# Kernel optimization log

Hardware: AMD Instinct MI355X
Metric: run time of the kernel (lower is better)

The kernel has to match this reference:

```python
import jax, jax.numpy as jnp
import numpy as np

B, T, N, H = 1024, 256, 32, 64  # batch, SEQ_LEN, N_SERIES, RNN_HID_SIZE
EPS = 1e-05


def setup_inputs() -> dict:
    key = jax.random.key(0)
    ks = jax.random.split(key, 24)
    s_h = 1.0 / np.sqrt(H)
    s_n = 1.0 / np.sqrt(N)
    u = lambda k, shape, s: jax.random.uniform(k, shape, jnp.float32, -s, s)
    inp = {
        'values': jax.random.normal(ks[0], (B, T, N), jnp.float32),
        'masks': (jax.random.uniform(ks[1], (B, T, N)) < 0.8).astype(jnp.float32),
        'deltas': jax.random.uniform(ks[2], (B, T, N), jnp.float32) * 5.0,
        'evals': jax.random.normal(ks[3], (B, T, N), jnp.float32),
        'eval_masks': (jax.random.uniform(ks[4], (B, T, N)) < 0.1).astype(jnp.float32),
        'labels': (jax.random.uniform(ks[5], (B, 1)) < 0.5).astype(jnp.float32),
        'is_train': jnp.ones((B, 1), jnp.float32),
        # TemporalDecay h: Linear(N->H)
        'td_h_W': u(ks[6], (H, N), s_h), 'td_h_b': u(ks[7], (H,), s_h),
        # TemporalDecay x: diag Linear(N->N)
        'td_x_W': u(ks[8], (N, N), s_n), 'td_x_b': u(ks[9], (N,), s_n),
        # hist_reg: Linear(H->N)
        'hist_W': u(ks[10], (N, H), s_n), 'hist_b': u(ks[11], (N,), s_n),
        # feat_reg: masked Linear(N->N), mask = 1 - I
        'feat_W': u(ks[12], (N, N), s_n), 'feat_b': u(ks[13], (N,), s_n),
        # weight_combine: Linear(2N->N)
        'wc_W': u(ks[14], (N, 2 * N), s_n), 'wc_b': u(ks[15], (N,), s_n),
        # LSTMCell(2N -> H)
        'W_ih': u(ks[16], (4 * H, 2 * N), s_h), 'W_hh': u(ks[17], (4 * H, H), s_h),
        'b_ih': u(ks[18], (4 * H,), s_h), 'b_hh': u(ks[19], (4 * H,), s_h),
        # out: Linear(H->1)
        'out_W': u(ks[20], (1, H), s_h), 'out_b': u(ks[21], (1,), s_h),
    }
    return inp


def _rits_forward(values, masks, deltas, labels, is_train,
                  td_h_W, td_h_b, td_x_W, td_x_b, hist_W, hist_b,
                  feat_W, feat_b, wc_W, wc_b, W_ih, W_hh, b_ih, b_hh,
                  out_W, out_b):
    # time-major for scan: [T, B, N]
    vals_t = jnp.swapaxes(values, 0, 1)
    masks_t = jnp.swapaxes(masks, 0, 1)
    delts_t = jnp.swapaxes(deltas, 0, 1)

    feat_mask = 1.0 - jnp.eye(N, dtype=values.dtype)
    td_x_diag = jnp.diagonal(td_x_W)                  # W * eye(N) linear == elementwise diag

    def step(carry, xmd):
        h, c, x_loss = carry
        x, m, d = xmd
        gamma_h = jnp.exp(-jax.nn.relu(d @ td_h_W.T + td_h_b))   # [B,H]
        gamma_x = jnp.exp(-jax.nn.relu(d * td_x_diag + td_x_b))  # [B,N]
        h = h * gamma_h
        x_h = h @ hist_W.T + hist_b
        msum = jnp.sum(m) + EPS
        x_loss = x_loss + jnp.sum(jnp.abs(x - x_h) * m) / msum
        x_c = m * x + (1.0 - m) * x_h
        z_h = x_c @ (feat_W * feat_mask).T + feat_b
        x_loss = x_loss + jnp.sum(jnp.abs(x - z_h) * m) / msum
        alpha = jnp.concatenate([gamma_x, m], axis=1) @ wc_W.T + wc_b
        c_h = alpha * z_h + (1.0 - alpha) * x_h
        x_loss = x_loss + jnp.sum(jnp.abs(x - c_h) * m) / msum
        c_c = m * x + (1.0 - m) * c_h
        inputs = jnp.concatenate([c_c, m], axis=1)  # [B, 2N]
        gates = inputs @ W_ih.T + b_ih + h @ W_hh.T + b_hh
        i, f, g, o = jnp.split(gates, 4, axis=1)
        c = jax.nn.sigmoid(f) * c + jax.nn.sigmoid(i) * jnp.tanh(g)
        h = jax.nn.sigmoid(o) * jnp.tanh(c)
        return (h, c, x_loss), c_c

    h0 = jnp.zeros((values.shape[0], H), values.dtype)
    c0 = jnp.zeros((values.shape[0], H), values.dtype)
    (h, c, x_loss), imps = jax.lax.scan(step, (h0, c0, jnp.float32(0.0)),
                                        (vals_t, masks_t, delts_t))
    imputations = jnp.swapaxes(imps, 0, 1)  # [B, T, N]

    y_h = h @ out_W.T + out_b  # logits [B,1]
    # binary_cross_entropy_with_logits, reduce=False
    max_val = jnp.maximum(-y_h, 0.0)
    bce = y_h - y_h * labels + max_val + jnp.log(jnp.exp(-max_val) + jnp.exp(-y_h - max_val))
    y_loss = jnp.sum(bce * is_train) / (jnp.sum(is_train) + EPS)
    loss = x_loss / T + y_loss * 0.1
    predictions = jax.nn.sigmoid(y_h)
    return loss, predictions, imputations


def reference(values, masks, deltas, evals, eval_masks, labels, is_train,
              td_h_W, td_h_b, td_x_W, td_x_b, hist_W, hist_b, feat_W, feat_b,
              wc_W, wc_b, W_ih, W_hh, b_ih, b_hh, out_W, out_b):
    loss, predictions, imputations = _rits_forward(
        values, masks, deltas, labels, is_train,
        td_h_W, td_h_b, td_x_W, td_x_b, hist_W, hist_b,
        feat_W, feat_b, wc_W, wc_b, W_ih, W_hh, b_ih, b_hh, out_W, out_b)
    return loss, predictions, imputations
```

## Files before the change

kernel.cpp:

```cpp
#include <hip/hip_runtime.h>

#define EPSF 1e-5f

typedef _Float16 h2f  __attribute__((ext_vector_type(2)));
typedef _Float16 h8   __attribute__((ext_vector_type(8)));
typedef float    f32x4 __attribute__((ext_vector_type(4)));

#if defined(__has_builtin)
#if __has_builtin(__builtin_amdgcn_fdot2)
#define HAVE_FDOT2 1
#endif
#endif

__device__ __forceinline__ float fsig(float x){ return 1.0f/(1.0f+__expf(-x)); }
__device__ __forceinline__ float ftanh(float x){
  float e = __expf(2.f*x);
  float r = (e-1.f)/(e+1.f);
  return (x > 15.f) ? 1.f : ((x < -15.f) ? -1.f : r);
}
__device__ __forceinline__ int pkf(float lo, float hi){
  return __builtin_bit_cast(int, __builtin_amdgcn_cvt_pkrtz(lo, hi));
}
__device__ __forceinline__ int4 mk4(const float* p){
  return make_int4(pkf(p[0],p[1]),pkf(p[2],p[3]),pkf(p[4],p[5]),pkf(p[6],p[7]));
}
__device__ __forceinline__ float dot2(int w, int x, float acc){
#ifdef HAVE_FDOT2
  return __builtin_amdgcn_fdot2(__builtin_bit_cast(h2f, w),
                                __builtin_bit_cast(h2f, x), acc, false);
#else
  h2f a = __builtin_bit_cast(h2f, w), b = __builtin_bit_cast(h2f, x);
  return acc + (float)a[0]*(float)b[0] + (float)a[1]*(float)b[1];
#endif
}
__device__ __forceinline__ int rl_i(int v, int l){ return __builtin_amdgcn_readlane(v, l); }
__device__ __forceinline__ float rl_f(float v, int l){
  return __int_as_float(__builtin_amdgcn_readlane(__float_as_int(v), l));
}
#define MFMA(A,B,C) __builtin_amdgcn_mfma_f32_16x16x32_f16( \
    __builtin_bit_cast(h8,(A)), __builtin_bit_cast(h8,(B)), (C), 0,0,0)
#define BAR() do{ asm volatile("s_waitcnt lgkmcnt(0)" ::: "memory"); __builtin_amdgcn_s_barrier(); }while(0)

__global__ void msum_kernel(const float* __restrict__ masks, float* __restrict__ msum){
  const int t   = blockIdx.x;
  const int tid = threadIdx.x;
  const int b0  = tid >> 3;
  const int n4  = (tid & 7) << 2;
  float s = 0.f;
  #pragma unroll 4
  for (int i = 0; i < 32; ++i) {
    const int b = b0 + (i << 5);
    const float4 v = *reinterpret_cast<const float4*>(masks + ((size_t)b*256 + t)*32 + n4);
    s += v.x + v.y + v.z + v.w;
  }
  __shared__ float red[256];
  red[tid] = s; __syncthreads();
  for (int off = 128; off > 0; off >>= 1) {
    if (tid < off) red[tid] += red[tid + off];
    __syncthreads();
  }
  if (tid == 0) msum[t] = red[0] + EPSF;
}

__global__ __launch_bounds__(512)
__attribute__((amdgpu_waves_per_eu(2, 2)))
void rits_kernel(
  const float* __restrict__ values, const float* __restrict__ masks,
  const float* __restrict__ deltas, const float* __restrict__ labels,
  const float* __restrict__ is_train,
  const float* __restrict__ td_h_W, const float* __restrict__ td_h_b,
  const float* __restrict__ td_x_W, const float* __restrict__ td_x_b,
  const float* __restrict__ hist_W, const float* __restrict__ hist_b,
  const float* __restrict__ feat_W, const float* __restrict__ feat_b,
  const float* __restrict__ wc_W,  const float* __restrict__ wc_b,
  const float* __restrict__ W_ih,  const float* __restrict__ W_hh,
  const float* __restrict__ b_ih,  const float* __restrict__ b_hh,
  const float* __restrict__ out_W, const float* __restrict__ out_b,
  const float* __restrict__ msum,
  float* __restrict__ xl_acc, float* __restrict__ bce_acc,
  float* __restrict__ predictions, float* __restrict__ imps)
{
  __shared__ __align__(16) int  inp_s[4][84];
  __shared__ __align__(16) int  dw_s[4][20];
  __shared__ float sB[4][64];
  __shared__ float gp[4][256];
  __shared__ float msum_l[256];

  const int tid = threadIdx.x;
  const int b   = blockIdx.x;
  const int wv  = tid >> 6;
  const int ln  = tid & 63;
  const bool chain = (wv < 4);
  const int me  = wv & 3;
  const int b2  = (b << 2) | me;
  const int kg  = ln >> 4;
  const int arow = ln & 15;

  if (tid < 256) msum_l[tid] = 1.0f / msum[tid];

  int4 Wb[2][4];
  #pragma unroll
  for (int nt = 0; nt < 2; ++nt){
    const int col = (wv << 5) + (nt << 4) + (ln & 15);
    #pragma unroll
    for (int ks = 0; ks < 4; ++ks){
      const int k0 = (ks << 5) + (kg << 3);
      const float* src = (k0 < 64) ? (W_ih + (size_t)col*64 + k0)
                                   : (W_hh + (size_t)col*64 + (k0 - 64));
      Wb[nt][ks] = make_int4(pkf(src[0],src[1]), pkf(src[2],src[3]),
                             pkf(src[4],src[5]), pkf(src[6],src[7]));
    }
  }
  const int col0 = (wv << 5) + (ln & 15);
  const float bs0 = b_ih[col0]      + b_hh[col0];
  const float bs1 = b_ih[col0 + 16] + b_hh[col0 + 16];

  int4 fGh = make_int4(0,0,0,0);
  float ghb = 0.f; int colj = 0;
  if (wv >= 4){
    colj = ((wv - 4) << 4) | (ln & 15);
    fGh  = mk4(td_h_W + colj*32 + kg*8);
    ghb  = td_h_b[colj];
  }

  int4  fC[8];
  int4  fDa[8];
  float wz[32];
  float tdxd_r=0.f, tdxb_r=0.f, histb_r=0.f, featb_r=0.f, wcb_r=0.f;
  float xv=0.f, mv=0.f, dv=0.f;
  if (chain){
    const int nr = ln & 31;
    #pragma unroll
    for (int g = 0; g < 8; ++g) fC[g] = mk4(hist_W + nr*64 + 8*g);
    #pragma unroll
    for (int g = 0; g < 8; ++g) fDa[g] = mk4(wc_W + nr*64 + 8*g);
    #pragma unroll
    for (int k = 0; k < 32; ++k) wz[k] = (k==nr) ? 0.f : feat_W[nr*32 + k];
    if (ln < 32){
      tdxd_r  = td_x_W[ln*33];
      tdxb_r  = td_x_b[ln];
      histb_r = hist_b[ln];
      featb_r = feat_b[ln];
      wcb_r   = wc_b[ln];
      const size_t base = (size_t)b2*8192 + ln;
      xv = values[base]; mv = masks[base]; dv = deltas[base];
    }
  }
  float h_reg = 0.f, c_reg = 0.f, loss_acc = 0.f;
  const int i0 = (2*ln) & 63, i1 = (2*ln+1) & 63;
  const int j0 = (2*ln-32) & 63, j1 = (2*ln-31) & 63;

  __syncthreads();

  if (chain){
    const int dwn = pkf(__shfl(dv, i0), __shfl(dv, i1));
    if (ln < 16) dw_s[me][ln] = dwn;
  }
  __syncthreads();
  if (wv >= 4){
    int4 A = make_int4(0,0,0,0);
    if (arow < 4) A = *reinterpret_cast<const int4*>(&dw_s[arow][kg << 2]);
    f32x4 acc = {ghb, ghb, ghb, ghb};
    acc = MFMA(A, fGh, acc);
    if (kg == 0){
      #pragma unroll
      for (int e = 0; e < 4; ++e) sB[e][colj] = acc[e];
    }
  }
  __syncthreads();

  for (int t = 0; t < 256; ++t){
    if (chain){
      const float x_cur = xv, m_cur = mv, d_cur = dv;
      const float sb = sB[me][ln];
      float gx_r = 0.f;
      if (ln < 32){
        gx_r = __expf(-fmaxf(fmaf(d_cur, tdxd_r, tdxb_r), 0.f));
        if (t < 255){
          const size_t base = (size_t)b2*8192 + (size_t)(t+1)*32 + ln;
          xv = values[base]; mv = masks[base]; dv = deltas[base];
        }
      }
      const float ga  = __shfl(gx_r,  i0), gb_ = __shfl(gx_r,  i1);
      const float ma_ = __shfl(m_cur, j0), mb_ = __shfl(m_cur, j1);
      const int aw = (ln < 16) ? pkf(ga, gb_) : pkf(ma_, mb_);

      h_reg *= __expf(-fmaxf(sb, 0.f));
      const int hw = pkf(__shfl(h_reg, i0), __shfl(h_reg, i1));
      float xh_v = 0.f, x_c_v = 0.f;
      if (ln < 32){
        float a0 = histb_r, a1 = 0.f, a2 = 0.f, a3 = 0.f;
        #pragma unroll
        for (int g4 = 0; g4 < 8; ++g4){
          const int4 w = fC[g4];
          a0 = dot2(w.x, rl_i(hw, 4*g4+0), a0);
          a1 = dot2(w.y, rl_i(hw, 4*g4+1), a1);
          a2 = dot2(w.z, rl_i(hw, 4*g4+2), a2);
          a3 = dot2(w.w, rl_i(hw, 4*g4+3), a3);
        }
        xh_v  = (a0+a1)+(a2+a3);
        x_c_v = m_cur*x_cur + (1.f-m_cur)*xh_v;
      }
      float ccv = 0.f;
      if (ln < 32){
        float z0 = featb_r, z1 = 0.f, z2 = 0.f, z3 = 0.f;
        #pragma unroll
        for (int k = 0; k < 32; k += 4){
          z0 = fmaf(rl_f(x_c_v, k+0), wz[k+0], z0);
          z1 = fmaf(rl_f(x_c_v, k+1), wz[k+1], z1);
          z2 = fmaf(rl_f(x_c_v, k+2), wz[k+2], z2);
          z3 = fmaf(rl_f(x_c_v, k+3), wz[k+3], z3);
        }
        const float z = (z0+z1)+(z2+z3);
        float a0 = wcb_r, a1 = 0.f, a2 = 0.f, a3 = 0.f;
        #pragma unroll
        for (int g4 = 0; g4 < 8; ++g4){
          const int4 w = fDa[g4];
          a0 = dot2(w.x, rl_i(aw, 4*g4+0), a0);
          a1 = dot2(w.y, rl_i(aw, 4*g4+1), a1);
          a2 = dot2(w.z, rl_i(aw, 4*g4+2), a2);
          a3 = dot2(w.w, rl_i(aw, 4*g4+3), a3);
        }
        const float al = (a0+a1)+(a2+a3);
        const float ch = al*z + (1.f-al)*xh_v;
        loss_acc += (fabsf(x_cur-xh_v)+fabsf(x_cur-z)+fabsf(x_cur-ch))*m_cur*msum_l[t];
        ccv = m_cur*x_cur + (1.f-m_cur)*ch;
        imps[(size_t)b2*8192 + (size_t)t*32 + ln] = ccv;
      }
      const int ccw = pkf(__shfl(ccv, i0), __shfl(ccv, i1));
      inp_s[me][ln] = (ln < 16) ? ccw : (ln < 32 ? aw : hw);
      if (t < 255){
        const int dwn = pkf(__shfl(dv, i0), __shfl(dv, i1));
        if (ln < 16) dw_s[me][ln] = dwn;
      }
    }

    BAR();

    {
      int4 A[4];
      if (arow < 4){
        #pragma unroll
        for (int ks = 0; ks < 4; ++ks)
          A[ks] = *reinterpret_cast<const int4*>(&inp_s[arow][(ks << 4) + (kg << 2)]);
      } else {
        #pragma unroll
        for (int ks = 0; ks < 4; ++ks) A[ks] = make_int4(0,0,0,0);
      }
      f32x4 acc0 = {bs0, bs0, bs0, bs0};
      f32x4 acc1 = {bs1, bs1, bs1, bs1};
      #pragma unroll
      for (int ks = 0; ks < 4; ++ks){
        acc0 = __builtin_amdgcn_mfma_f32_16x16x32_f16(
                 __builtin_bit_cast(h8, A[ks]), __builtin_bit_cast(h8, Wb[0][ks]), acc0, 0,0,0);
        acc1 = __builtin_amdgcn_mfma_f32_16x16x32_f16(
                 __builtin_bit_cast(h8, A[ks]), __builtin_bit_cast(h8, Wb[1][ks]), acc1, 0,0,0);
      }
      if (kg == 0){
        #pragma unroll
        for (int e = 0; e < 4; ++e){
          gp[e][col0]      = acc0[e];
          gp[e][col0 + 16] = acc1[e];
        }
      }
    }
    if (wv >= 4){
      int4 Agh = make_int4(0,0,0,0);
      if (arow < 4) Agh = *reinterpret_cast<const int4*>(&dw_s[arow][kg << 2]);
      f32x4 accg = {ghb, ghb, ghb, ghb};
      accg = MFMA(Agh, fGh, accg);
      if (kg == 0){
        #pragma unroll
        for (int e = 0; e < 4; ++e) sB[e][colj] = accg[e];
      }
    }

    BAR();

    if (chain){
      const float ig = gp[me][ln];
      const float fg = gp[me][64+ln];
      const float gg = gp[me][128+ln];
      const float og = gp[me][192+ln];
      c_reg = fsig(fg)*c_reg + fsig(ig)*ftanh(gg);
      h_reg = fsig(og)*ftanh(c_reg);
    }
  }

  if (chain){
    float l = loss_acc;
    l += __shfl_xor(l,16); l += __shfl_xor(l,8);
    l += __shfl_xor(l,4);  l += __shfl_xor(l,2); l += __shfl_xor(l,1);
    if (ln == 0) atomicAdd(xl_acc, l);

    float p = h_reg * out_W[ln];
    p += __shfl_xor(p,32); p += __shfl_xor(p,16); p += __shfl_xor(p,8);
    p += __shfl_xor(p,4);  p += __shfl_xor(p,2);  p += __shfl_xor(p,1);
    if (ln == 0){
      const float y = p + out_b[0];
      predictions[b2] = fsig(y);
      const float lab = labels[b2];
      const float it  = is_train[b2];
      const float mx  = fmaxf(-y, 0.f);
      const float bce = y - y*lab + mx + __logf(__expf(-mx) + __expf(-y - mx));
      atomicAdd(bce_acc, bce * it);
    }
  }
}

__global__ void final_kernel(const float* __restrict__ is_train,
                             const float* __restrict__ ws,
                             float* __restrict__ out){
  const int tid = threadIdx.x;
  __shared__ float red[256];
  red[tid] = is_train[tid] + is_train[tid+256] + is_train[tid+512] + is_train[tid+768];
  __syncthreads();
  for (int off = 128; off > 0; off >>= 1){
    if (tid < off) red[tid] += red[tid + off];
    __syncthreads();
  }
  if (tid == 0){
    const float yl = ws[1] / (red[0] + EPSF);
    out[0] = ws[0] / 256.0f + 0.1f * yl;
  }
}

extern "C" void kernel_launch(void* const* d_in, const int* in_sizes, int n_in,
                              void* d_out, int out_size, void* d_ws, size_t ws_size,
                              hipStream_t stream){
  const float* values   = (const float*)d_in[0];
  const float* masks    = (const float*)d_in[1];
  const float* deltas   = (const float*)d_in[2];
  const float* labels   = (const float*)d_in[5];
  const float* is_train = (const float*)d_in[6];
  const float* td_h_W   = (const float*)d_in[7];
  const float* td_h_b   = (const float*)d_in[8];
  const float* td_x_W   = (const float*)d_in[9];
  const float* td_x_b   = (const float*)d_in[10];
  const float* hist_W   = (const float*)d_in[11];
  const float* hist_b   = (const float*)d_in[12];
  const float* feat_W   = (const float*)d_in[13];
  const float* feat_b   = (const float*)d_in[14];
  const float* wc_W     = (const float*)d_in[15];
  const float* wc_b     = (const float*)d_in[16];
  const float* W_ih     = (const float*)d_in[17];
  const float* W_hh     = (const float*)d_in[18];
  const float* b_ih     = (const float*)d_in[19];
  const float* b_hh     = (const float*)d_in[20];
  const float* out_W    = (const float*)d_in[21];
  const float* out_b    = (const float*)d_in[22];

  float* out = (float*)d_out;
  float* ws  = (float*)d_ws;

  hipMemsetAsync(ws, 0, 2*sizeof(float), stream);
  msum_kernel<<<256, 256, 0, stream>>>(masks, ws + 2);
  rits_kernel<<<256, 512, 0, stream>>>(values, masks, deltas, labels, is_train,
      td_h_W, td_h_b, td_x_W, td_x_b, hist_W, hist_b, feat_W, feat_b,
      wc_W, wc_b, W_ih, W_hh, b_ih, b_hh, out_W, out_b,
      ws + 2, ws + 0, ws + 1, out + 1, out + 1 + 1024);
  final_kernel<<<1, 256, 0, stream>>>(is_train, ws, out);
}
```

Before: 441.7 us.

## Precompute weight-combine alpha for next step on helper waves via MFMA

The weight_combine linear (alpha from gamma_x and mask) depends only on inputs, not on the recurrent state. It is moved off the serial chain waves, which used per-lane dot2 loops, onto helper waves 4-5. Those waves compute it one step ahead with MFMA, alongside the temporal-decay MFMA, and pass the result through shared memory. This shortens the critical per-step chain and frees the fDa registers, at the cost of extra shared-memory traffic and more work in the helper waves.

Measured after the change: 434.7 us. Within noise of the previous version (-1.6%).

```diff
diff --git a/kernel.cpp b/kernel.cpp
--- a/kernel.cpp
+++ b/kernel.cpp
@@ -81,8 +81,9 @@
   float* __restrict__ predictions, float* __restrict__ imps)
 {
   __shared__ __align__(16) int  inp_s[4][84];
-  __shared__ __align__(16) int  dw_s[4][20];
+  __shared__ __align__(16) int  nb[4][52];
   __shared__ float sB[4][64];
+  __shared__ float sAl[4][32];
   __shared__ float gp[4][256];
   __shared__ float msum_l[256];
 
@@ -117,23 +118,28 @@
 
   int4 fGh = make_int4(0,0,0,0);
   float ghb = 0.f; int colj = 0;
+  int4 fA0 = make_int4(0,0,0,0), fA1 = make_int4(0,0,0,0);
+  float alb = 0.f; int colA = 0;
   if (wv >= 4){
     colj = ((wv - 4) << 4) | (ln & 15);
     fGh  = mk4(td_h_W + colj*32 + kg*8);
     ghb  = td_h_b[colj];
+    if (wv < 6){
+      colA = ((wv - 4) << 4) | (ln & 15);
+      fA0  = mk4(wc_W + colA*64 + kg*8);
+      fA1  = mk4(wc_W + colA*64 + 32 + kg*8);
+      alb  = wc_b[colA];
+    }
   }
 
   int4  fC[8];
-  int4  fDa[8];
   float wz[32];
-  float tdxd_r=0.f, tdxb_r=0.f, histb_r=0.f, featb_r=0.f, wcb_r=0.f;
+  float tdxd_r=0.f, tdxb_r=0.f, histb_r=0.f, featb_r=0.f;
   float xv=0.f, mv=0.f, dv=0.f;
   if (chain){
     const int nr = ln & 31;
     #pragma unroll
     for (int g = 0; g < 8; ++g) fC[g] = mk4(hist_W + nr*64 + 8*g);
-    #pragma unroll
-    for (int g = 0; g < 8; ++g) fDa[g] = mk4(wc_W + nr*64 + 8*g);
     #pragma unroll
     for (int k = 0; k < 32; ++k) wz[k] = (k==nr) ? 0.f : feat_W[nr*32 + k];
     if (ln < 32){
@@ -141,7 +147,6 @@
       tdxb_r  = td_x_b[ln];
       histb_r = hist_b[ln];
       featb_r = feat_b[ln];
-      wcb_r   = wc_b[ln];
       const size_t base = (size_t)b2*8192 + ln;
       xv = values[base]; mv = masks[base]; dv = deltas[base];
     }
@@ -153,37 +158,51 @@
   __syncthreads();
 
   if (chain){
-    const int dwn = pkf(__shfl(dv, i0), __shfl(dv, i1));
-    if (ln < 16) dw_s[me][ln] = dwn;
+    float gx0 = 0.f;
+    if (ln < 32) gx0 = __expf(-fmaxf(fmaf(dv, tdxd_r, tdxb_r), 0.f));
+    const int dw0 = pkf(__shfl(dv,  i0), __shfl(dv,  i1));
+    const int gw0 = pkf(__shfl(gx0, i0), __shfl(gx0, i1));
+    const int mw0 = pkf(__shfl(mv,  i0), __shfl(mv,  i1));
+    if (ln < 16){ nb[me][ln]=dw0; nb[me][16+ln]=gw0; nb[me][32+ln]=mw0; }
   }
   __syncthreads();
   if (wv >= 4){
     int4 A = make_int4(0,0,0,0);
-    if (arow < 4) A = *reinterpret_cast<const int4*>(&dw_s[arow][kg << 2]);
+    if (arow < 4) A = *reinterpret_cast<const int4*>(&nb[arow][kg << 2]);
     f32x4 acc = {ghb, ghb, ghb, ghb};
     acc = MFMA(A, fGh, acc);
     if (kg == 0){
       #pragma unroll
       for (int e = 0; e < 4; ++e) sB[e][colj] = acc[e];
     }
+    if (wv < 6){
+      int4 A0 = make_int4(0,0,0,0), A1 = make_int4(0,0,0,0);
+      if (arow < 4){
+        A0 = *reinterpret_cast<const int4*>(&nb[arow][16 + (kg << 2)]);
+        A1 = *reinterpret_cast<const int4*>(&nb[arow][32 + (kg << 2)]);
+      }
+      f32x4 aacc = {alb, alb, alb, alb};
+      aacc = MFMA(A0, fA0, aacc);
+      aacc = MFMA(A1, fA1, aacc);
+      if (kg == 0){
+        #pragma unroll
+        for (int e = 0; e < 4; ++e) sAl[e][colA] = aacc[e];
+      }
+    }
   }
   __syncthreads();
 
   for (int t = 0; t < 256; ++t){
     if (chain){
-      const float x_cur = xv, m_cur = mv, d_cur = dv;
+      const float x_cur = xv, m_cur = mv;
       const float sb = sB[me][ln];
-      float gx_r = 0.f;
-      if (ln < 32){
-        gx_r = __expf(-fmaxf(fmaf(d_cur, tdxd_r, tdxb_r), 0.f));
-        if (t < 255){
-          const size_t base = (size_t)b2*8192 + (size_t)(t+1)*32 + ln;
-          xv = values[base]; mv = masks[base]; dv = deltas[base];
-        }
-      }
-      const float ga  = __shfl(gx_r,  i0), gb_ = __shfl(gx_r,  i1);
+      const float al = (ln < 32) ? sAl[me][ln] : 0.f;
+      if (ln < 32 && t < 255){
+        const size_t base = (size_t)b2*8192 + (size_t)(t+1)*32 + ln;
+        xv = values[base]; mv = masks[base]; dv = deltas[base];
+      }
       const float ma_ = __shfl(m_cur, j0), mb_ = __shfl(m_cur, j1);
-      const int aw = (ln < 16) ? pkf(ga, gb_) : pkf(ma_, mb_);
+      const int mwc = pkf(ma_, mb_);
 
       h_reg *= __expf(-fmaxf(sb, 0.f));
       const int hw = pkf(__shfl(h_reg, i0), __shfl(h_reg, i1));
@@ -212,26 +231,20 @@
           z3 = fmaf(rl_f(x_c_v, k+3), wz[k+3], z3);
         }
         const float z = (z0+z1)+(z2+z3);
-        float a0 = wcb_r, a1 = 0.f, a2 = 0.f, a3 = 0.f;
-        #pragma unroll
-        for (int g4 = 0; g4 < 8; ++g4){
-          const int4 w = fDa[g4];
-          a0 = dot2(w.x, rl_i(aw, 4*g4+0), a0);
-          a1 = dot2(w.y, rl_i(aw, 4*g4+1), a1);
-          a2 = dot2(w.z, rl_i(aw, 4*g4+2), a2);
-          a3 = dot2(w.w, rl_i(aw, 4*g4+3), a3);
-        }
-        const float al = (a0+a1)+(a2+a3);
         const float ch = al*z + (1.f-al)*xh_v;
         loss_acc += (fabsf(x_cur-xh_v)+fabsf(x_cur-z)+fabsf(x_cur-ch))*m_cur*msum_l[t];
         ccv = m_cur*x_cur + (1.f-m_cur)*ch;
         imps[(size_t)b2*8192 + (size_t)t*32 + ln] = ccv;
       }
       const int ccw = pkf(__shfl(ccv, i0), __shfl(ccv, i1));
-      inp_s[me][ln] = (ln < 16) ? ccw : (ln < 32 ? aw : hw);
-      if (t < 255){
-        const int dwn = pkf(__shfl(dv, i0), __shfl(dv, i1));
-        if (ln < 16) dw_s[me][ln] = dwn;
+      inp_s[me][ln] = (ln < 16) ? ccw : (ln < 32 ? mwc : hw);
+      {
+        float gxn = 0.f;
+        if (ln < 32) gxn = __expf(-fmaxf(fmaf(dv, tdxd_r, tdxb_r), 0.f));
+        const int dwn = pkf(__shfl(dv,  i0), __shfl(dv,  i1));
+        const int gwn = pkf(__shfl(gxn, i0), __shfl(gxn, i1));
+        const int mwn = pkf(__shfl(mv,  i0), __shfl(mv,  i1));
+        if (ln < 16){ nb[me][ln]=dwn; nb[me][16+ln]=gwn; nb[me][32+ln]=mwn; }
       }
     }
 
@@ -266,12 +279,26 @@
     }
     if (wv >= 4){
       int4 Agh = make_int4(0,0,0,0);
-      if (arow < 4) Agh = *reinterpret_cast<const int4*>(&dw_s[arow][kg << 2]);
+      if (arow < 4) Agh = *reinterpret_cast<const int4*>(&nb[arow][kg << 2]);
       f32x4 accg = {ghb, ghb, ghb, ghb};
       accg = MFMA(Agh, fGh, accg);
       if (kg == 0){
         #pragma unroll
         for (int e = 0; e < 4; ++e) sB[e][colj] = accg[e];
+      }
+      if (wv < 6){
+        int4 A0 = make_int4(0,0,0,0), A1 = make_int4(0,0,0,0);
+        if (arow < 4){
+          A0 = *reinterpret_cast<const int4*>(&nb[arow][16 + (kg << 2)]);
+          A1 = *reinterpret_cast<const int4*>(&nb[arow][32 + (kg << 2)]);
+        }
+        f32x4 aacc = {alb, alb, alb, alb};
+        aacc = MFMA(A0, fA0, aacc);
+        aacc = MFMA(A1, fA1, aacc);
+        if (kg == 0){
+          #pragma unroll
+          for (int e = 0; e < 4; ++e) sAl[e][colA] = aacc[e];
+        }
       }
     }
 
```
